# Optimization experiments

Measured on AMD Instinct MI355X. Metric: run time of the kernel, lower is better.

The kernel has to match this reference:

```python
import jax, jax.numpy as jnp
import numpy as np

NEG_SLOPE = 0.2


def gat_layer(x, src, dst, W, a_src, a_dst, b, heads, ch):
    """PyG-style GATConv (self-loops already appended to src/dst)."""
    N = x.shape[0]
    h = (x @ W).reshape(N, heads, ch)                 # [N,H,C]
    alpha_s = (h * a_src).sum(-1)                      # [N,H]
    alpha_d = (h * a_dst).sum(-1)                      # [N,H]
    e = jax.nn.leaky_relu(alpha_s[src] + alpha_d[dst], NEG_SLOPE)  # [E,H]
    # segment softmax over edges grouped by destination node
    m = jax.ops.segment_max(e, dst, num_segments=N)    # [N,H]
    ex = jnp.exp(e - m[dst])
    s = jax.ops.segment_sum(ex, dst, num_segments=N)   # [N,H]
    a = ex / (s[dst] + 1e-16)                          # [E,H]
    out = jax.ops.segment_sum(h[src] * a[:, :, None], dst, num_segments=N)  # [N,H,C]
    return out.reshape(N, heads * ch) + b


def setup_inputs() -> dict:
    key = jax.random.key(0)
    ks = jax.random.split(key, 12)
    N, E = 20000, 320000
    IN, HID, HEADS, OUT = 3, 64, 4, 21
    x = jax.random.normal(ks[0], (N, IN), dtype=jnp.float32)
    edge_index = jax.random.randint(ks[1], (2, E), 0, N, dtype=jnp.int32)
    g = 1.0 / np.sqrt(HID)
    inp = {
        "x": x,
        "edge_index": edge_index,
        "W1": jax.random.normal(ks[2], (IN, HEADS * HID), dtype=jnp.float32) * (1.0 / np.sqrt(IN)),
        "att_src1": jax.random.normal(ks[3], (HEADS, HID), dtype=jnp.float32) * g,
        "att_dst1": jax.random.normal(ks[4], (HEADS, HID), dtype=jnp.float32) * g,
        "b1": jnp.zeros((HEADS * HID,), dtype=jnp.float32),
        "W2": jax.random.normal(ks[5], (HEADS * HID, OUT), dtype=jnp.float32) * (1.0 / np.sqrt(HEADS * HID)),
        "att_src2": jax.random.normal(ks[6], (1, OUT), dtype=jnp.float32) * (1.0 / np.sqrt(OUT)),
        "att_dst2": jax.random.normal(ks[7], (1, OUT), dtype=jnp.float32) * (1.0 / np.sqrt(OUT)),
        "b2": jnp.zeros((OUT,), dtype=jnp.float32),
    }
    return inp


def reference(x, edge_index, W1, att_src1, att_dst1, b1, W2, att_src2, att_dst2, b2):
    N = x.shape[0]
    loop = jnp.arange(N, dtype=edge_index.dtype)
    src = jnp.concatenate([edge_index[0], loop])
    dst = jnp.concatenate([edge_index[1], loop])
    h = gat_layer(x, src, dst, W1, att_src1, att_dst1, b1, heads=4, ch=64)
    h = jax.nn.relu(h)
    h = gat_layer(h, src, dst, W2, att_src2, att_dst2, b2, heads=1, ch=21)
    return jax.nn.softmax(h, axis=1)
```

## Files before the change

kernel.cpp:

```cpp
#include <hip/hip_runtime.h>

#define HID   256
#define HEADS 4
#define OUT_C 21
#define H2S   24
#define NEG_SLOPE 0.2f
#define CAP   64
#define CAPSH 6


__global__ void alpha_zero_kernel(const float* __restrict__ x, const float* __restrict__ W1,
                                  const float* __restrict__ a_s, const float* __restrict__ a_d,
                                  float4* __restrict__ pxs, float4* __restrict__ ad1,
                                  int* __restrict__ cursor, int N) {
    __shared__ float wa[24];
    int t = threadIdx.x;
    int head = t >> 6;
    float avs = a_s[t], avd = a_d[t];
#pragma unroll
    for (int k = 0; k < 3; ++k) {
        float w = W1[k * HID + t];
        float ps = w * avs, pd = w * avd;
        for (int m = 32; m >= 1; m >>= 1) {
            ps += __shfl_xor(ps, m);
            pd += __shfl_xor(pd, m);
        }
        if ((t & 63) == 0) {
            wa[k * HEADS + head] = ps;
            wa[12 + k * HEADS + head] = pd;
        }
    }
    __syncthreads();
    int n = blockIdx.x * 256 + t;
    if (n >= N) return;
    cursor[n] = 0;
    float x0 = x[n * 3], x1 = x[n * 3 + 1], x2 = x[n * 3 + 2];
    float s[HEADS], d[HEADS];
#pragma unroll
    for (int h = 0; h < HEADS; ++h) {
        s[h] = x0 * wa[h] + x1 * wa[4 + h] + x2 * wa[8 + h];
        d[h] = x0 * wa[12 + h] + x1 * wa[16 + h] + x2 * wa[20 + h];
    }
    pxs[2 * n]     = make_float4(x0, x1, x2, s[0]);
    pxs[2 * n + 1] = make_float4(s[1], s[2], s[3], 0.f);
    ad1[n] = make_float4(d[0], d[1], d[2], d[3]);
}


__global__ void scatter_count_kernel(const int* __restrict__ ei, int E, int N,
                                     int* __restrict__ cursor, int* __restrict__ table) {
    int i = blockIdx.x * blockDim.x + threadIdx.x;
    int Eh = E >> 1;
    if (i < Eh) {
        int2 s2 = ((const int2*)ei)[i];
        int2 d2 = ((const int2*)(ei + E))[i];
        int p0 = atomicAdd(&cursor[d2.x], 1);
        if (p0 < CAP) table[(d2.x << CAPSH) + p0] = s2.x;
        int p1 = atomicAdd(&cursor[d2.y], 1);
        if (p1 < CAP) table[(d2.y << CAPSH) + p1] = s2.y;
    } else {
        int n = i - Eh;
        if (n < N) {
            int p = atomicAdd(&cursor[n], 1);
            if (p < CAP) table[(n << CAPSH) + p] = n;
        } else if ((E & 1) && n == N) {
            int src = ei[E - 1], dst = ei[2 * E - 1];
            int p = atomicAdd(&cursor[dst], 1);
            if (p < CAP) table[(dst << CAPSH) + p] = src;
        }
    }
}


__global__ void aggr_node_kernel(const int* __restrict__ cursor, const int* __restrict__ table,
                                 const float4* __restrict__ pxs, const float4* __restrict__ ad1,
                                 const float* __restrict__ W1, const float* __restrict__ b1,
                                 const float* __restrict__ W2, const float* __restrict__ a2s,
                                 const float* __restrict__ a2d, float* __restrict__ h2p,
                                 int N) {
    __shared__ float4 wc[HID];
    __shared__ float  w2s[HID * H2S];
    int tid = threadIdx.x;
    {
        int k = tid;
        wc[k] = make_float4(W1[k], W1[HID + k], W1[2 * HID + k], b1[k]);
        for (int idx = tid; idx < HID * OUT_C; idx += 256) {
            int k2 = idx / OUT_C;
            int o = idx - k2 * OUT_C;
            w2s[k2 * H2S + o] = W2[idx];
        }
    }
    __syncthreads();
    int g = blockIdx.x * 256 + tid;
    int n = g >> 3;
    int sub = g & 7;
    if (n >= N) return;

    float4 adv = ad1[n];
    float ad[HEADS] = {adv.x, adv.y, adv.z, adv.w};
    float sum[HEADS] = {0, 0, 0, 0};
    float s0[HEADS] = {0, 0, 0, 0}, s1[HEADS] = {0, 0, 0, 0}, s2[HEADS] = {0, 0, 0, 0};
    int deg = min(cursor[n], CAP);
    const int* row = table + ((size_t)n << CAPSH);
    int j = sub;
    int s_next = row[j < deg ? j : 0];
    float4 A_next = pxs[2 * s_next];
    float4 B_next = pxs[2 * s_next + 1];
    while (j < deg) {
        float4 A = A_next, B = B_next;
        int jn = j + 8;
        s_next = row[jn < deg ? jn : 0];
        A_next = pxs[2 * s_next];
        B_next = pxs[2 * s_next + 1];
        float a[HEADS] = {A.w, B.x, B.y, B.z};
#pragma unroll
        for (int h = 0; h < HEADS; ++h) {
            float e = a[h] + ad[h];
            e = (e > 0.f) ? e : NEG_SLOPE * e;
            float p = __expf(e);
            sum[h] += p;
            s0[h] = fmaf(p, A.x, s0[h]);
            s1[h] = fmaf(p, A.y, s1[h]);
            s2[h] = fmaf(p, A.z, s2[h]);
        }
        j = jn;
    }
#pragma unroll
    for (int h = 0; h < HEADS; ++h) {
        s0[h] += __shfl_xor(s0[h], 1);  s0[h] += __shfl_xor(s0[h], 2);  s0[h] += __shfl_xor(s0[h], 4);
        s1[h] += __shfl_xor(s1[h], 1);  s1[h] += __shfl_xor(s1[h], 2);  s1[h] += __shfl_xor(s1[h], 4);
        s2[h] += __shfl_xor(s2[h], 1);  s2[h] += __shfl_xor(s2[h], 2);  s2[h] += __shfl_xor(s2[h], 4);
        sum[h] += __shfl_xor(sum[h], 1); sum[h] += __shfl_xor(sum[h], 2); sum[h] += __shfl_xor(sum[h], 4);
    }

    float acc[OUT_C];
#pragma unroll
    for (int o = 0; o < OUT_C; ++o) acc[o] = 0.f;
#pragma unroll
    for (int h = 0; h < HEADS; ++h) {
        float gx = s0[h], gy = s1[h], gz = s2[h];
        float gi = 1.0f / (sum[h] + 1e-16f);
#pragma unroll
        for (int i2 = 0; i2 < 8; ++i2) {
            int k = h * 64 + i2 * 8 + sub;
            float4 w = wc[k];
            float r = fmaf(fmaf(gx, w.x, fmaf(gy, w.y, gz * w.z)), gi, w.w);
            r = fmaxf(r, 0.f);
            const float4* wr = (const float4*)&w2s[k * H2S];
            float4 w0 = wr[0], w1 = wr[1], w2v = wr[2], w3 = wr[3], w4 = wr[4];
            float w20 = w2s[k * H2S + 20];
            acc[0]  = fmaf(r, w0.x, acc[0]);   acc[1]  = fmaf(r, w0.y, acc[1]);
            acc[2]  = fmaf(r, w0.z, acc[2]);   acc[3]  = fmaf(r, w0.w, acc[3]);
            acc[4]  = fmaf(r, w1.x, acc[4]);   acc[5]  = fmaf(r, w1.y, acc[5]);
            acc[6]  = fmaf(r, w1.z, acc[6]);   acc[7]  = fmaf(r, w1.w, acc[7]);
            acc[8]  = fmaf(r, w2v.x, acc[8]);  acc[9]  = fmaf(r, w2v.y, acc[9]);
            acc[10] = fmaf(r, w2v.z, acc[10]); acc[11] = fmaf(r, w2v.w, acc[11]);
            acc[12] = fmaf(r, w3.x, acc[12]);  acc[13] = fmaf(r, w3.y, acc[13]);
            acc[14] = fmaf(r, w3.z, acc[14]);  acc[15] = fmaf(r, w3.w, acc[15]);
            acc[16] = fmaf(r, w4.x, acc[16]);  acc[17] = fmaf(r, w4.y, acc[17]);
            acc[18] = fmaf(r, w4.z, acc[18]);  acc[19] = fmaf(r, w4.w, acc[19]);
            acc[20] = fmaf(r, w20, acc[20]);
        }
    }
#pragma unroll
    for (int o = 0; o < OUT_C; ++o) {
        acc[o] += __shfl_xor(acc[o], 1);
        acc[o] += __shfl_xor(acc[o], 2);
        acc[o] += __shfl_xor(acc[o], 4);
    }
    if (sub == 0) {
        float s = 0.f, d = 0.f;
#pragma unroll
        for (int o = 0; o < OUT_C; ++o) {
            s = fmaf(acc[o], a2s[o], s);
            d = fmaf(acc[o], a2d[o], d);
        }
        float4* hv = (float4*)&h2p[n * H2S];
        hv[0] = make_float4(acc[0], acc[1], acc[2], acc[3]);
        hv[1] = make_float4(acc[4], acc[5], acc[6], acc[7]);
        hv[2] = make_float4(acc[8], acc[9], acc[10], acc[11]);
        hv[3] = make_float4(acc[12], acc[13], acc[14], acc[15]);
        hv[4] = make_float4(acc[16], acc[17], acc[18], acc[19]);
        hv[5] = make_float4(acc[20], s, d, 0.f);
    }
}


__global__ void l2_aggr_kernel(const int* __restrict__ cursor, const int* __restrict__ table,
                               const float* __restrict__ h2p, const float* __restrict__ b2,
                               float* __restrict__ out, int N) {
    __shared__ float part[2][44];
    int tid = threadIdx.x;
    int wave = tid >> 6;
    int lane = tid & 63;
    int slot = wave >> 1;
    int w2 = wave & 1;
    int n = blockIdx.x * 2 + slot;
    bool an = (n < N);
    int nn = an ? n : 0;

    int lgrp = lane / 21;
    int c = lane - lgrp * 21;
    bool ingrp = (lgrp < 3) && an;
    int grp = w2 * 3 + lgrp;
    int deg = an ? min(cursor[nn], CAP) : 0;
    const int* row = table + ((size_t)nn << CAPSH);
    float ad = h2p[nn * H2S + 22];

    int j = grp;
    bool v0 = ingrp && (j < deg);
    int si0 = row[v0 ? j : 0];
    float a0 = h2p[si0 * H2S + 21];
    float vv0 = h2p[si0 * H2S + c];
    j += 6;
    bool v1 = ingrp && (j < deg);
    int si1 = row[v1 ? j : 0];

    float accv = 0.f, sump = 0.f;
    int iters = (deg + 5) / 6;
    for (int it = 0; it < iters; ++it) {
        float a1 = h2p[si1 * H2S + 21];
        float vv1 = h2p[si1 * H2S + c];
        j += 6;
        bool v2 = ingrp && (j < deg);
        int si2 = row[v2 ? j : 0];
        float e = a0 + ad;
        e = (e > 0.f) ? e : NEG_SLOPE * e;
        float p = v0 ? __expf(e) : 0.f;
        sump += p;
        accv = fmaf(p, vv0, accv);
        a0 = a1; vv0 = vv1; v0 = v1; v1 = v2; si1 = si2;
    }
    float acc_t = accv + __shfl(accv, lane + 21) + __shfl(accv, lane + 42);
    float sum_t = __shfl(sump, 0) + __shfl(sump, 21) + __shfl(sump, 42);
    if (lane < OUT_C) part[slot][w2 * 22 + lane] = acc_t;
    if (lane == 0)    part[slot][w2 * 22 + 21] = sum_t;
    __syncthreads();
    if (w2 == 0) {
        float accT = (lane < OUT_C) ? (part[slot][lane] + part[slot][22 + lane]) : 0.f;
        float sumT = part[slot][21] + part[slot][43];
        float o = (lane < OUT_C) ? (accT / (sumT + 1e-16f) + b2[lane]) : -1e30f;
        float mx = o;
        for (int m = 16; m >= 1; m >>= 1) mx = fmaxf(mx, __shfl_xor(mx, m));
        float ex = (lane < OUT_C) ? __expf(o - mx) : 0.f;
        float tot = ex;
        for (int m = 16; m >= 1; m >>= 1) tot += __shfl_xor(tot, m);
        if (an && lane < OUT_C) out[n * OUT_C + lane] = ex / tot;
    }
}


extern "C" void kernel_launch(void* const* d_in, const int* in_sizes, int n_in,
                              void* d_out, int out_size, void* d_ws, size_t ws_size,
                              hipStream_t stream) {
    const float* x     = (const float*)d_in[0];
    const int*   ei    = (const int*)d_in[1];
    const float* W1    = (const float*)d_in[2];
    const float* asrc1 = (const float*)d_in[3];
    const float* adst1 = (const float*)d_in[4];
    const float* b1    = (const float*)d_in[5];
    const float* W2    = (const float*)d_in[6];
    const float* asrc2 = (const float*)d_in[7];
    const float* adst2 = (const float*)d_in[8];
    const float* b2    = (const float*)d_in[9];
    float* out = (float*)d_out;

    const int N = in_sizes[0] / 3;
    const int E = in_sizes[1] / 2;

    size_t off = 0;
    auto alloc = [&](size_t bytes) -> char* {
        off = (off + 255) & ~(size_t)255;
        char* p = (char*)d_ws + off;
        off += bytes;
        return p;
    };
    int*    cursor = (int*)alloc((size_t)N * 4);
    int*    table  = (int*)alloc((size_t)N * CAP * 4);
    float4* pxs    = (float4*)alloc((size_t)N * 32);
    float4* ad1    = (float4*)alloc((size_t)N * 16);
    float*  h2p    = (float*)alloc((size_t)N * H2S * 4);
    (void)ws_size;

    alpha_zero_kernel<<<(N + 255) / 256, 256, 0, stream>>>(x, W1, asrc1, adst1,
                                                           pxs, ad1, cursor, N);
    int sthreads = (E >> 1) + N + (E & 1);
    scatter_count_kernel<<<(sthreads + 255) / 256, 256, 0, stream>>>(ei, E, N, cursor, table);

    aggr_node_kernel<<<(8 * N + 255) / 256, 256, 0, stream>>>(cursor, table, pxs, ad1,
                                                              W1, b1, W2, asrc2, adst2,
                                                              h2p, N);
    l2_aggr_kernel<<<(N + 1) / 2, 256, 0, stream>>>(cursor, table, h2p, b2, out, N);
}
```

Baseline: 131.4 us.

## Process two nodes per 8-lane group in layer-1 and one wave per node in layer-2

The layer-1 fused aggregation now gives each 8-lane group two destination nodes, 4 lanes gathering edges for each. The 256x21 projection then runs once per pair with two accumulator sets, so the shared-memory W2 reads are amortized over two nodes and the grid is halved. The layer-2 aggregation drops the two-wave-per-node split with its shared-memory partials and __syncthreads, using one wave per node with 3 edge groups. This cuts projection-weight traffic and block syncs, at the cost of more registers per lane and fewer lanes gathering each node's edges.

```diff
diff --git a/kernel.cpp b/kernel.cpp
--- a/kernel.cpp
+++ b/kernel.cpp
@@ -7,7 +7,6 @@
 #define NEG_SLOPE 0.2f
 #define CAP   64
 #define CAPSH 6
-
 
 __global__ void alpha_zero_kernel(const float* __restrict__ x, const float* __restrict__ W1,
                                   const float* __restrict__ a_s, const float* __restrict__ a_d,
@@ -45,7 +44,6 @@
     pxs[2 * n + 1] = make_float4(s[1], s[2], s[3], 0.f);
     ad1[n] = make_float4(d[0], d[1], d[2], d[3]);
 }
-
 
 __global__ void scatter_count_kernel(const int* __restrict__ ei, int E, int N,
                                      int* __restrict__ cursor, int* __restrict__ table) {
@@ -71,7 +69,6 @@
     }
 }
 
-
 __global__ void aggr_node_kernel(const int* __restrict__ cursor, const int* __restrict__ table,
                                  const float4* __restrict__ pxs, const float4* __restrict__ ad1,
                                  const float* __restrict__ W1, const float* __restrict__ b1,
@@ -92,23 +89,30 @@
     }
     __syncthreads();
     int g = blockIdx.x * 256 + tid;
-    int n = g >> 3;
-    int sub = g & 7;
-    if (n >= N) return;
-
-    float4 adv = ad1[n];
+    int grp = g >> 3;
+    int gl = g & 7;
+    int nA = grp * 2;
+    int nB = nA + 1;
+    if (nA >= N) return;
+    bool isB = (gl >= 4);
+    int n_mine = isB ? nB : nA;
+    bool active = (n_mine < N);
+    int nm = active ? n_mine : nA;
+
+    int sub = gl & 3;
+    float4 adv = ad1[nm];
     float ad[HEADS] = {adv.x, adv.y, adv.z, adv.w};
     float sum[HEADS] = {0, 0, 0, 0};
     float s0[HEADS] = {0, 0, 0, 0}, s1[HEADS] = {0, 0, 0, 0}, s2[HEADS] = {0, 0, 0, 0};
-    int deg = min(cursor[n], CAP);
-    const int* row = table + ((size_t)n << CAPSH);
+    int deg = active ? min(cursor[nm], CAP) : 0;
+    const int* row = table + ((size_t)nm << CAPSH);
     int j = sub;
     int s_next = row[j < deg ? j : 0];
     float4 A_next = pxs[2 * s_next];
     float4 B_next = pxs[2 * s_next + 1];
     while (j < deg) {
         float4 A = A_next, B = B_next;
-        int jn = j + 8;
+        int jn = j + 4;
         s_next = row[jn < deg ? jn : 0];
         A_next = pxs[2 * s_next];
         B_next = pxs[2 * s_next + 1];
@@ -127,101 +131,139 @@
     }
 #pragma unroll
     for (int h = 0; h < HEADS; ++h) {
-        s0[h] += __shfl_xor(s0[h], 1);  s0[h] += __shfl_xor(s0[h], 2);  s0[h] += __shfl_xor(s0[h], 4);
-        s1[h] += __shfl_xor(s1[h], 1);  s1[h] += __shfl_xor(s1[h], 2);  s1[h] += __shfl_xor(s1[h], 4);
-        s2[h] += __shfl_xor(s2[h], 1);  s2[h] += __shfl_xor(s2[h], 2);  s2[h] += __shfl_xor(s2[h], 4);
-        sum[h] += __shfl_xor(sum[h], 1); sum[h] += __shfl_xor(sum[h], 2); sum[h] += __shfl_xor(sum[h], 4);
-    }
-
-    float acc[OUT_C];
-#pragma unroll
-    for (int o = 0; o < OUT_C; ++o) acc[o] = 0.f;
+        s0[h] += __shfl_xor(s0[h], 1);   s0[h] += __shfl_xor(s0[h], 2);
+        s1[h] += __shfl_xor(s1[h], 1);   s1[h] += __shfl_xor(s1[h], 2);
+        s2[h] += __shfl_xor(s2[h], 1);   s2[h] += __shfl_xor(s2[h], 2);
+        sum[h] += __shfl_xor(sum[h], 1); sum[h] += __shfl_xor(sum[h], 2);
+    }
+    float As0[HEADS], As1[HEADS], As2[HEADS], Ai[HEADS];
+    float Bs0[HEADS], Bs1[HEADS], Bs2[HEADS], Bi[HEADS];
 #pragma unroll
     for (int h = 0; h < HEADS; ++h) {
-        float gx = s0[h], gy = s1[h], gz = s2[h];
-        float gi = 1.0f / (sum[h] + 1e-16f);
+        float o0 = __shfl_xor(s0[h], 4);
+        float o1 = __shfl_xor(s1[h], 4);
+        float o2 = __shfl_xor(s2[h], 4);
+        float ow = __shfl_xor(sum[h], 4);
+        As0[h] = isB ? o0 : s0[h];   Bs0[h] = isB ? s0[h] : o0;
+        As1[h] = isB ? o1 : s1[h];   Bs1[h] = isB ? s1[h] : o1;
+        As2[h] = isB ? o2 : s2[h];   Bs2[h] = isB ? s2[h] : o2;
+        float aw = isB ? ow : sum[h];
+        float bw = isB ? sum[h] : ow;
+        Ai[h] = 1.0f / (aw + 1e-16f);
+        Bi[h] = 1.0f / (bw + 1e-16f);
+    }
+
+    float accA[OUT_C], accB[OUT_C];
+#pragma unroll
+    for (int o = 0; o < OUT_C; ++o) { accA[o] = 0.f; accB[o] = 0.f; }
+#pragma unroll
+    for (int h = 0; h < HEADS; ++h) {
+        float gax = As0[h], gay = As1[h], gaz = As2[h], gai = Ai[h];
+        float gbx = Bs0[h], gby = Bs1[h], gbz = Bs2[h], gbi = Bi[h];
 #pragma unroll
         for (int i2 = 0; i2 < 8; ++i2) {
-            int k = h * 64 + i2 * 8 + sub;
+            int k = h * 64 + i2 * 8 + gl;
             float4 w = wc[k];
-            float r = fmaf(fmaf(gx, w.x, fmaf(gy, w.y, gz * w.z)), gi, w.w);
-            r = fmaxf(r, 0.f);
+            float rA = fmaf(fmaf(gax, w.x, fmaf(gay, w.y, gaz * w.z)), gai, w.w);
+            float rB = fmaf(fmaf(gbx, w.x, fmaf(gby, w.y, gbz * w.z)), gbi, w.w);
+            rA = fmaxf(rA, 0.f);
+            rB = fmaxf(rB, 0.f);
             const float4* wr = (const float4*)&w2s[k * H2S];
             float4 w0 = wr[0], w1 = wr[1], w2v = wr[2], w3 = wr[3], w4 = wr[4];
             float w20 = w2s[k * H2S + 20];
-            acc[0]  = fmaf(r, w0.x, acc[0]);   acc[1]  = fmaf(r, w0.y, acc[1]);
-            acc[2]  = fmaf(r, w0.z, acc[2]);   acc[3]  = fmaf(r, w0.w, acc[3]);
-            acc[4]  = fmaf(r, w1.x, acc[4]);   acc[5]  = fmaf(r, w1.y, acc[5]);
-            acc[6]  = fmaf(r, w1.z, acc[6]);   acc[7]  = fmaf(r, w1.w, acc[7]);
-            acc[8]  = fmaf(r, w2v.x, acc[8]);  acc[9]  = fmaf(r, w2v.y, acc[9]);
-            acc[10] = fmaf(r, w2v.z, acc[10]); acc[11] = fmaf(r, w2v.w, acc[11]);
-            acc[12] = fmaf(r, w3.x, acc[12]);  acc[13] = fmaf(r, w3.y, acc[13]);
-            acc[14] = fmaf(r, w3.z, acc[14]);  acc[15] = fmaf(r, w3.w, acc[15]);
-            acc[16] = fmaf(r, w4.x, acc[16]);  acc[17] = fmaf(r, w4.y, acc[17]);
-            acc[18] = fmaf(r, w4.z, acc[18]);  acc[19] = fmaf(r, w4.w, acc[19]);
-            acc[20] = fmaf(r, w20, acc[20]);
+            accA[0]  = fmaf(rA, w0.x, accA[0]);   accB[0]  = fmaf(rB, w0.x, accB[0]);
+            accA[1]  = fmaf(rA, w0.y, accA[1]);   accB[1]  = fmaf(rB, w0.y, accB[1]);
+            accA[2]  = fmaf(rA, w0.z, accA[2]);   accB[2]  = fmaf(rB, w0.z, accB[2]);
+            accA[3]  = fmaf(rA, w0.w, accA[3]);   accB[3]  = fmaf(rB, w0.w, accB[3]);
+            accA[4]  = fmaf(rA, w1.x, accA[4]);   accB[4]  = fmaf(rB, w1.x, accB[4]);
+            accA[5]  = fmaf(rA, w1.y, accA[5]);   accB[5]  = fmaf(rB, w1.y, accB[5]);
+            accA[6]  = fmaf(rA, w1.z, accA[6]);   accB[6]  = fmaf(rB, w1.z, accB[6]);
+            accA[7]  = fmaf(rA, w1.w, accA[7]);   accB[7]  = fmaf(rB, w1.w, accB[7]);
+            accA[8]  = fmaf(rA, w2v.x, accA[8]);  accB[8]  = fmaf(rB, w2v.x, accB[8]);
+            accA[9]  = fmaf(rA, w2v.y, accA[9]);  accB[9]  = fmaf(rB, w2v.y, accB[9]);
+            accA[10] = fmaf(rA, w2v.z, accA[10]); accB[10] = fmaf(rB, w2v.z, accB[10]);
+            accA[11] = fmaf(rA, w2v.w, accA[11]); accB[11] = fmaf(rB, w2v.w, accB[11]);
+            accA[12] = fmaf(rA, w3.x, accA[12]);  accB[12] = fmaf(rB, w3.x, accB[12]);
+            accA[13] = fmaf(rA, w3.y, accA[13]);  accB[13] = fmaf(rB, w3.y, accB[13]);
+            accA[14] = fmaf(rA, w3.z, accA[14]);  accB[14] = fmaf(rB, w3.z, accB[14]);
+            accA[15] = fmaf(rA, w3.w, accA[15]);  accB[15] = fmaf(rB, w3.w, accB[15]);
+            accA[16] = fmaf(rA, w4.x, accA[16]);  accB[16] = fmaf(rB, w4.x, accB[16]);
+            accA[17] = fmaf(rA, w4.y, accA[17]);  accB[17] = fmaf(rB, w4.y, accB[17]);
+            accA[18] = fmaf(rA, w4.z, accA[18]);  accB[18] = fmaf(rB, w4.z, accB[18]);
+            accA[19] = fmaf(rA, w4.w, accA[19]);  accB[19] = fmaf(rB, w4.w, accB[19]);
+            accA[20] = fmaf(rA, w20, accA[20]);   accB[20] = fmaf(rB, w20, accB[20]);
         }
     }
 #pragma unroll
     for (int o = 0; o < OUT_C; ++o) {
-        acc[o] += __shfl_xor(acc[o], 1);
-        acc[o] += __shfl_xor(acc[o], 2);
-        acc[o] += __shfl_xor(acc[o], 4);
-    }
-    if (sub == 0) {
+        accA[o] += __shfl_xor(accA[o], 1);
+        accA[o] += __shfl_xor(accA[o], 2);
+        accA[o] += __shfl_xor(accA[o], 4);
+        accB[o] += __shfl_xor(accB[o], 1);
+        accB[o] += __shfl_xor(accB[o], 2);
+        accB[o] += __shfl_xor(accB[o], 4);
+    }
+    if (gl == 0) {
         float s = 0.f, d = 0.f;
 #pragma unroll
         for (int o = 0; o < OUT_C; ++o) {
-            s = fmaf(acc[o], a2s[o], s);
-            d = fmaf(acc[o], a2d[o], d);
-        }
-        float4* hv = (float4*)&h2p[n * H2S];
-        hv[0] = make_float4(acc[0], acc[1], acc[2], acc[3]);
-        hv[1] = make_float4(acc[4], acc[5], acc[6], acc[7]);
-        hv[2] = make_float4(acc[8], acc[9], acc[10], acc[11]);
-        hv[3] = make_float4(acc[12], acc[13], acc[14], acc[15]);
-        hv[4] = make_float4(acc[16], acc[17], acc[18], acc[19]);
-        hv[5] = make_float4(acc[20], s, d, 0.f);
-    }
-}
-
+            s = fmaf(accA[o], a2s[o], s);
+            d = fmaf(accA[o], a2d[o], d);
+        }
+        float4* hv = (float4*)&h2p[nA * H2S];
+        hv[0] = make_float4(accA[0], accA[1], accA[2], accA[3]);
+        hv[1] = make_float4(accA[4], accA[5], accA[6], accA[7]);
+        hv[2] = make_float4(accA[8], accA[9], accA[10], accA[11]);
+        hv[3] = make_float4(accA[12], accA[13], accA[14], accA[15]);
+        hv[4] = make_float4(accA[16], accA[17], accA[18], accA[19]);
+        hv[5] = make_float4(accA[20], s, d, 0.f);
+    }
+    if (gl == 4 && nB < N) {
+        float s = 0.f, d = 0.f;
+#pragma unroll
+        for (int o = 0; o < OUT_C; ++o) {
+            s = fmaf(accB[o], a2s[o], s);
+            d = fmaf(accB[o], a2d[o], d);
+        }
+        float4* hv = (float4*)&h2p[nB * H2S];
+        hv[0] = make_float4(accB[0], accB[1], accB[2], accB[3]);
+        hv[1] = make_float4(accB[4], accB[5], accB[6], accB[7]);
+        hv[2] = make_float4(accB[8], accB[9], accB[10], accB[11]);
+        hv[3] = make_float4(accB[12], accB[13], accB[14], accB[15]);
+        hv[4] = make_float4(accB[16], accB[17], accB[18], accB[19]);
+        hv[5] = make_float4(accB[20], s, d, 0.f);
+    }
+}
 
 __global__ void l2_aggr_kernel(const int* __restrict__ cursor, const int* __restrict__ table,
                                const float* __restrict__ h2p, const float* __restrict__ b2,
                                float* __restrict__ out, int N) {
-    __shared__ float part[2][44];
-    int tid = threadIdx.x;
-    int wave = tid >> 6;
-    int lane = tid & 63;
-    int slot = wave >> 1;
-    int w2 = wave & 1;
-    int n = blockIdx.x * 2 + slot;
-    bool an = (n < N);
-    int nn = an ? n : 0;
-
-    int lgrp = lane / 21;
-    int c = lane - lgrp * 21;
-    bool ingrp = (lgrp < 3) && an;
-    int grp = w2 * 3 + lgrp;
-    int deg = an ? min(cursor[nn], CAP) : 0;
-    const int* row = table + ((size_t)nn << CAPSH);
-    float ad = h2p[nn * H2S + 22];
+    int wave = threadIdx.x >> 6;
+    int lane = threadIdx.x & 63;
+    int n = blockIdx.x * 4 + wave;
+    if (n >= N) return;
+    int grp = lane / 21;
+    int c = lane - grp * 21;
+    bool ingrp = (grp < 3);
+    int deg = min(cursor[n], CAP);
+    const int* row = table + ((size_t)n << CAPSH);
+    int iters = (deg + 2) / 3;
+    float ad = h2p[n * H2S + 22];
 
     int j = grp;
     bool v0 = ingrp && (j < deg);
     int si0 = row[v0 ? j : 0];
     float a0 = h2p[si0 * H2S + 21];
     float vv0 = h2p[si0 * H2S + c];
-    j += 6;
+    j += 3;
     bool v1 = ingrp && (j < deg);
     int si1 = row[v1 ? j : 0];
 
     float accv = 0.f, sump = 0.f;
-    int iters = (deg + 5) / 6;
     for (int it = 0; it < iters; ++it) {
         float a1 = h2p[si1 * H2S + 21];
         float vv1 = h2p[si1 * H2S + c];
-        j += 6;
+        j += 3;
         bool v2 = ingrp && (j < deg);
         int si2 = row[v2 ? j : 0];
         float e = a0 + ad;
@@ -233,20 +275,13 @@
     }
     float acc_t = accv + __shfl(accv, lane + 21) + __shfl(accv, lane + 42);
     float sum_t = __shfl(sump, 0) + __shfl(sump, 21) + __shfl(sump, 42);
-    if (lane < OUT_C) part[slot][w2 * 22 + lane] = acc_t;
-    if (lane == 0)    part[slot][w2 * 22 + 21] = sum_t;
-    __syncthreads();
-    if (w2 == 0) {
-        float accT = (lane < OUT_C) ? (part[slot][lane] + part[slot][22 + lane]) : 0.f;
-        float sumT = part[slot][21] + part[slot][43];
-        float o = (lane < OUT_C) ? (accT / (sumT + 1e-16f) + b2[lane]) : -1e30f;
-        float mx = o;
-        for (int m = 16; m >= 1; m >>= 1) mx = fmaxf(mx, __shfl_xor(mx, m));
-        float ex = (lane < OUT_C) ? __expf(o - mx) : 0.f;
-        float tot = ex;
-        for (int m = 16; m >= 1; m >>= 1) tot += __shfl_xor(tot, m);
-        if (an && lane < OUT_C) out[n * OUT_C + lane] = ex / tot;
-    }
+    float o = (lane < OUT_C) ? (acc_t / (sum_t + 1e-16f) + b2[lane]) : -1e30f;
+    float mx = o;
+    for (int m = 16; m >= 1; m >>= 1) mx = fmaxf(mx, __shfl_xor(mx, m));
+    float ex = (lane < OUT_C) ? __expf(o - mx) : 0.f;
+    float tot = ex;
+    for (int m = 16; m >= 1; m >>= 1) tot += __shfl_xor(tot, m);
+    if (lane < OUT_C) out[n * OUT_C + lane] = ex / tot;
 }
 
 
@@ -287,8 +322,9 @@
     int sthreads = (E >> 1) + N + (E & 1);
     scatter_count_kernel<<<(sthreads + 255) / 256, 256, 0, stream>>>(ei, E, N, cursor, table);
 
-    aggr_node_kernel<<<(8 * N + 255) / 256, 256, 0, stream>>>(cursor, table, pxs, ad1,
-                                                              W1, b1, W2, asrc2, adst2,
-                                                              h2p, N);
-    l2_aggr_kernel<<<(N + 1) / 2, 256, 0, stream>>>(cursor, table, h2p, b2, out, N);
-}
+    int npairs = (N + 1) / 2;
+    aggr_node_kernel<<<(8 * npairs + 255) / 256, 256, 0, stream>>>(
+        cursor, table, pxs, ad1, W1, b1, W2, asrc2, adst2, h2p, N);
+
+    l2_aggr_kernel<<<(N + 3) / 4, 256, 0, stream>>>(cursor, table, h2p, b2, out, N);
+}
```

Measured after the change: 129.7 us. Within noise of the previous version (-1.4%).
